# Kernel tuning notes

Measured on AMD Instinct MI355X. Metric: run time of the kernel, lower is better.

Reference implementation:

```python
import jax, jax.numpy as jnp
import numpy as np

HEAD_DIM = 32
KERNEL = 3
DILATION = 2
PAD = DILATION * (KERNEL - 1) // 2  # 'same' padding for dilated window
SCALE = HEAD_DIM ** -0.5


def _unfold_windows(x):
    """x: [B, d, H, W] -> [B, d, k*k, H, W] dilated local windows.
    Matches torch nn.Unfold ordering: kernel row-major (i outer, j inner)."""
    B, d, H, W = x.shape
    xp = jnp.pad(x, ((0, 0), (0, 0), (PAD, PAD), (PAD, PAD)))
    taps = [xp[:, :, i * DILATION:i * DILATION + H, j * DILATION:j * DILATION + W]
            for i in range(KERNEL) for j in range(KERNEL)]  # fixed 9-tap loop
    return jnp.stack(taps, axis=2)


def setup_inputs() -> dict:
    key = jax.random.key(0)
    kq, kk, kv = jax.random.split(key, 3)
    shape = (16, 32, 128, 128)
    return {
        "q": jax.random.normal(kq, shape, dtype=jnp.float32),
        "k": jax.random.normal(kk, shape, dtype=jnp.float32),
        "v": jax.random.normal(kv, shape, dtype=jnp.float32),
    }


def reference(q, k, v):
    # k,v windows: [B, d, n, H, W] with n = kernel_size**2
    kw = _unfold_windows(k)
    vw = _unfold_windows(v)
    # per-pixel 1xN attention: scores [B, n, H, W]
    attn = jnp.einsum('bdhw,bdnhw->bnhw', q, kw) * SCALE
    attn = jax.nn.softmax(attn, axis=1)
    # weighted sum over window taps -> [B, d, H, W]
    return jnp.einsum('bnhw,bdnhw->bdhw', attn, vw)
```

## Files before the change

kernel.cpp:

```cpp
#include <hip/hip_runtime.h>


#define BB 16
#define HD 32
#define HH 128
#define WW 128
#define PLANE (HH * WW)
#define CHUNK 4

__global__ __launch_bounds__(128) void dilate_attn_kernel(
    const float* __restrict__ q,
    const float* __restrict__ k,
    const float* __restrict__ v,
    float* __restrict__ out)
{
    const int w   = threadIdx.x;
    const int bid = blockIdx.x;
    const int rowid = (bid & 7) * 256 + (bid >> 3);
    const int h = rowid & (HH - 1);
    const int b = rowid >> 7;

    const size_t base = ((size_t)b * HD) * PLANE + (size_t)h * WW + w;

    const int  dlo = (w >= 2)      ? -2      : -w;
    const int  dhi = (w <= WW - 3) ?  2      : (WW - 1 - w);
    const int  rlo = (h >= 2)      ? -2 * WW : 0;
    const int  rhi = (h <= HH - 3) ?  2 * WW : 0;
    const bool wlo = (w >= 2), whi = (w <= WW - 3);
    const bool hlo = (h >= 2), hhi = (h <= HH - 3);

    int off[9];
    off[0] = rlo + dlo; off[1] = rlo; off[2] = rlo + dhi;
    off[3] = dlo;       off[4] = 0;   off[5] = dhi;
    off[6] = rhi + dlo; off[7] = rhi; off[8] = rhi + dhi;

    const bool tv[9] = { hlo && wlo, hlo, hlo && whi,
                         wlo,        true, whi,
                         hhi && wlo, hhi, hhi && whi };

    float s[9];
    #pragma unroll
    for (int n = 0; n < 9; ++n) s[n] = 0.f;

    const float* qp = q + base;
    const float* kp = k + base;

    for (int dc = 0; dc < HD; dc += CHUNK) {
        float qreg[CHUNK];
        float kreg[CHUNK][9];
        #pragma unroll
        for (int u = 0; u < CHUNK; ++u) {
            const float* kc = kp + (size_t)(dc + u) * PLANE;
            qreg[u] = qp[(size_t)(dc + u) * PLANE];
            #pragma unroll
            for (int n = 0; n < 9; ++n) kreg[u][n] = kc[off[n]];
        }
        #pragma unroll
        for (int u = 0; u < CHUNK; ++u) {
            #pragma unroll
            for (int n = 0; n < 9; ++n)
                s[n] = fmaf(qreg[u], kreg[u][n], s[n]);
        }
    }

    #pragma unroll
    for (int n = 0; n < 9; ++n) if (!tv[n]) s[n] = 0.f;

    const float scale = 0.17677669529663687f;
    float m = -3.4e38f;
    #pragma unroll
    for (int n = 0; n < 9; ++n) { s[n] *= scale; m = fmaxf(m, s[n]); }
    float sum = 0.f;
    #pragma unroll
    for (int n = 0; n < 9; ++n) { s[n] = __expf(s[n] - m); sum += s[n]; }
    const float inv = 1.f / sum;
    #pragma unroll
    for (int n = 0; n < 9; ++n) s[n] *= inv;

    #pragma unroll
    for (int n = 0; n < 9; ++n) if (!tv[n]) s[n] = 0.f;

    const float* vp = v + base;
    float*       op = out + base;

    for (int dc = 0; dc < HD; dc += CHUNK) {
        float vreg[CHUNK][9];
        #pragma unroll
        for (int u = 0; u < CHUNK; ++u) {
            const float* vc = vp + (size_t)(dc + u) * PLANE;
            #pragma unroll
            for (int n = 0; n < 9; ++n) vreg[u][n] = vc[off[n]];
        }
        #pragma unroll
        for (int u = 0; u < CHUNK; ++u) {
            float acc = 0.f;
            #pragma unroll
            for (int n = 0; n < 9; ++n)
                acc = fmaf(s[n], vreg[u][n], acc);
            op[(size_t)(dc + u) * PLANE] = acc;
        }
    }
}

extern "C" void kernel_launch(void* const* d_in, const int* in_sizes, int n_in,
                              void* d_out, int out_size, void* d_ws, size_t ws_size,
                              hipStream_t stream) {
    const float* q = (const float*)d_in[0];
    const float* k = (const float*)d_in[1];
    const float* v = (const float*)d_in[2];
    float* out = (float*)d_out;

    dim3 grid(BB * HH);
    dim3 block(WW);
    dilate_attn_kernel<<<grid, block, 0, stream>>>(q, k, v, out);
}
```

Before: 34.31 us.

## Share dilated window columns across lanes via wave shuffles instead of redundant loads

Each thread now loads only its own column of the three k/v rows and computes partial dot products against shifted q columns. Horizontal neighbours are exchanged with cross-lane shuffles, and LDS plus a block barrier handle the edges between the two waves. This cuts global load instructions from 9 to 3 per channel for k, and replaces the v gathers with shuffles plus a small side load. The cost is extra q loads, shuffle instructions, a __syncthreads, and more complex edge handling.

New measurement: 35.64 us. +3.9%, slower.

```diff
diff --git a/kernel.cpp b/kernel.cpp
--- a/kernel.cpp
+++ b/kernel.cpp
@@ -14,53 +14,90 @@
     const float* __restrict__ v,
     float* __restrict__ out)
 {
-    const int w   = threadIdx.x;
-    const int bid = blockIdx.x;
+    __shared__ float ex_lo[2][3][2];
+    __shared__ float ex_hi[2][3][2];
+
+    const int tid  = threadIdx.x;
+    const int wave = tid >> 6;
+    const int lane = tid & 63;
+    const int w0   = wave << 6;
+    const int w    = tid;
+
+    const int bid   = blockIdx.x;
     const int rowid = (bid & 7) * 256 + (bid >> 3);
     const int h = rowid & (HH - 1);
     const int b = rowid >> 7;
 
-    const size_t base = ((size_t)b * HD) * PLANE + (size_t)h * WW + w;
+    const size_t base = (size_t)b * HD * PLANE + (size_t)h * WW;
 
-    const int  dlo = (w >= 2)      ? -2      : -w;
-    const int  dhi = (w <= WW - 3) ?  2      : (WW - 1 - w);
-    const int  rlo = (h >= 2)      ? -2 * WW : 0;
-    const int  rhi = (h <= HH - 3) ?  2 * WW : 0;
+    const bool hlo = (h >= 2), hhi = (h <= HH - 3);
+    const int  roff[3] = { hlo ? -2 * WW : 0, 0, hhi ? 2 * WW : 0 };
     const bool wlo = (w >= 2), whi = (w <= WW - 3);
-    const bool hlo = (h >= 2), hhi = (h <= HH - 3);
-
-    int off[9];
-    off[0] = rlo + dlo; off[1] = rlo; off[2] = rlo + dhi;
-    off[3] = dlo;       off[4] = 0;   off[5] = dhi;
-    off[6] = rhi + dlo; off[7] = rhi; off[8] = rhi + dhi;
-
     const bool tv[9] = { hlo && wlo, hlo, hlo && whi,
                          wlo,        true, whi,
                          hhi && wlo, hhi, hhi && whi };
 
-    float s[9];
-    #pragma unroll
-    for (int n = 0; n < 9; ++n) s[n] = 0.f;
+    const int cqm2 = wlo ? w - 2 : 0;
+    const int cqp2 = whi ? w + 2 : WW - 1;
 
-    const float* qp = q + base;
-    const float* kp = k + base;
+    int scol = w0;
+    if (lane < 2)        scol = w0 + lane - 2;
+    else if (lane >= 62) scol = w0 + lane + 2;
+    scol = scol < 0 ? 0 : (scol > WW - 1 ? WW - 1 : scol);
 
-    for (int dc = 0; dc < HD; dc += CHUNK) {
-        float qreg[CHUNK];
-        float kreg[CHUNK][9];
+    const int idxm2 = (lane >= 2) ? lane - 2 : 0;
+    const int idxp2 = (lane < 62) ? lane + 2 : 63;
+
+    float Plo[3] = {0.f, 0.f, 0.f};
+    float Pce[3] = {0.f, 0.f, 0.f};
+    float Phi[3] = {0.f, 0.f, 0.f};
+
+    const float* qrow = q + base;
+    const float* krow = k + base;
+
+    for (int c = 0; c < HD; c += CHUNK) {
+        float kr[CHUNK][3], q0[CHUNK], qm[CHUNK], qp[CHUNK];
         #pragma unroll
         for (int u = 0; u < CHUNK; ++u) {
-            const float* kc = kp + (size_t)(dc + u) * PLANE;
-            qreg[u] = qp[(size_t)(dc + u) * PLANE];
-            #pragma unroll
-            for (int n = 0; n < 9; ++n) kreg[u][n] = kc[off[n]];
+            const size_t dp = (size_t)(c + u) * PLANE;
+            kr[u][0] = krow[dp + roff[0] + w];
+            kr[u][1] = krow[dp + w];
+            kr[u][2] = krow[dp + roff[2] + w];
+            q0[u]    = qrow[dp + w];
+            qm[u]    = qrow[dp + cqm2];
+            qp[u]    = qrow[dp + cqp2];
         }
         #pragma unroll
         for (int u = 0; u < CHUNK; ++u) {
             #pragma unroll
-            for (int n = 0; n < 9; ++n)
-                s[n] = fmaf(qreg[u], kreg[u][n], s[n]);
+            for (int r = 0; r < 3; ++r) {
+                Plo[r] = fmaf(qp[u], kr[u][r], Plo[r]);
+                Pce[r] = fmaf(q0[u], kr[u][r], Pce[r]);
+                Phi[r] = fmaf(qm[u], kr[u][r], Phi[r]);
+            }
         }
+    }
+
+    if (lane < 2) {
+        #pragma unroll
+        for (int r = 0; r < 3; ++r) ex_hi[wave][r][lane] = Phi[r];
+    }
+    if (lane >= 62) {
+        #pragma unroll
+        for (int r = 0; r < 3; ++r) ex_lo[wave][r][lane - 62] = Plo[r];
+    }
+    __syncthreads();
+
+    float s[9];
+    #pragma unroll
+    for (int r = 0; r < 3; ++r) {
+        float slo = __shfl(Plo[r], idxm2);
+        if (lane < 2)  slo = ex_lo[wave ^ 1][r][lane];
+        float shi = __shfl(Phi[r], idxp2);
+        if (lane >= 62) shi = ex_hi[wave ^ 1][r][lane - 62];
+        s[r * 3 + 0] = slo;
+        s[r * 3 + 1] = Pce[r];
+        s[r * 3 + 2] = shi;
     }
 
     #pragma unroll
@@ -80,24 +117,34 @@
     #pragma unroll
     for (int n = 0; n < 9; ++n) if (!tv[n]) s[n] = 0.f;
 
-    const float* vp = v + base;
-    float*       op = out + base;
+    const float* vrow = v + base;
+    float*       orow = out + base;
 
-    for (int dc = 0; dc < HD; dc += CHUNK) {
-        float vreg[CHUNK][9];
+    for (int c = 0; c < HD; c += CHUNK) {
+        float vce[CHUNK][3], vsm[CHUNK][3];
         #pragma unroll
         for (int u = 0; u < CHUNK; ++u) {
-            const float* vc = vp + (size_t)(dc + u) * PLANE;
+            const size_t dp = (size_t)(c + u) * PLANE;
             #pragma unroll
-            for (int n = 0; n < 9; ++n) vreg[u][n] = vc[off[n]];
+            for (int r = 0; r < 3; ++r) {
+                vce[u][r] = vrow[dp + roff[r] + w];
+                vsm[u][r] = vrow[dp + roff[r] + scol];
+            }
         }
         #pragma unroll
         for (int u = 0; u < CHUNK; ++u) {
             float acc = 0.f;
             #pragma unroll
-            for (int n = 0; n < 9; ++n)
-                acc = fmaf(s[n], vreg[u][n], acc);
-            op[(size_t)(dc + u) * PLANE] = acc;
+            for (int r = 0; r < 3; ++r) {
+                float vlo = __shfl(vce[u][r], idxm2);
+                vlo = (lane < 2) ? vsm[u][r] : vlo;
+                float vhi = __shfl(vce[u][r], idxp2);
+                vhi = (lane >= 62) ? vsm[u][r] : vhi;
+                acc = fmaf(s[r * 3 + 0], vlo,       acc);
+                acc = fmaf(s[r * 3 + 1], vce[u][r], acc);
+                acc = fmaf(s[r * 3 + 2], vhi,       acc);
+            }
+            orow[(size_t)(c + u) * PLANE + w] = acc;
         }
     }
 }
```
